# Optimization experiments

Hardware: AMD Instinct MI355X
Metric: run time of the kernel (lower is better)

Reference implementation:

```python
import jax, jax.numpy as jnp
import numpy as np

NH = 8      # num_heads
AG = 49     # agent_num
PS = 7      # pool_size = sqrt(agent_num)


def _pool_mat(in_size, out_size):
    # torch AdaptiveAvgPool2d bin boundaries: start=floor(i*n/o), end=ceil((i+1)*n/o)
    P = np.zeros((out_size, in_size), dtype=np.float32)
    for i in range(out_size):
        s = (i * in_size) // out_size
        e = -((-(i + 1) * in_size) // out_size)
        P[i, s:e] = 1.0 / (e - s)
    return jnp.asarray(P)


def setup_inputs() -> dict:
    key = jax.random.key(0)
    ks = jax.random.split(key, 16)
    b, n, dim, ic, cc = 32, 1024, 512, 512, 256
    s = 0.02
    d = {}
    d['x'] = jax.random.normal(ks[0], (b, n, dim), jnp.float32)
    d['context'] = jax.random.normal(ks[1], (b, n, cc), jnp.float32)
    d['Wq'] = jax.random.normal(ks[2], (dim, ic), jnp.float32) * s
    d['Wkv'] = jax.random.normal(ks[3], (dim, 2 * ic), jnp.float32) * s
    d['conv_w'] = jax.random.normal(ks[4], (ic, ic + cc, 3, 3), jnp.float32) * s
    d['conv_b'] = jnp.zeros((ic,), jnp.float32)
    d['dwc_w'] = jax.random.normal(ks[5], (ic, 1, 3, 3), jnp.float32) * s
    d['dwc_b'] = jnp.zeros((ic,), jnp.float32)
    d['proj_w'] = jax.random.normal(ks[6], (ic, dim), jnp.float32) * s
    d['proj_b'] = jnp.zeros((dim,), jnp.float32)
    d['an_bias'] = jax.random.normal(ks[7], (NH, AG, 7, 7), jnp.float32) * s
    d['na_bias'] = jax.random.normal(ks[8], (NH, AG, 7, 7), jnp.float32) * s
    d['ah_bias'] = jax.random.normal(ks[9], (1, NH, AG, 32, 1), jnp.float32) * s
    d['aw_bias'] = jax.random.normal(ks[10], (1, NH, AG, 1, 32), jnp.float32) * s
    d['ha_bias'] = jax.random.normal(ks[11], (1, NH, 32, 1, AG), jnp.float32) * s
    d['wa_bias'] = jax.random.normal(ks[12], (1, NH, 1, 32, AG), jnp.float32) * s
    d['H'] = 32; d['W'] = 32; d['c_H'] = 32; d['c_W'] = 32
    return d


def reference(x, context, Wq, Wkv, conv_w, conv_b, dwc_w, dwc_b, proj_w, proj_b,
              an_bias, na_bias, ah_bias, aw_bias, ha_bias, wa_bias, H, W, c_H, c_W):
    b, n, _ = x.shape
    ic = Wq.shape[1]
    cc = context.shape[-1]
    nh, ag = NH, AG
    hd = ic // nh
    scale = hd ** -0.5

    q = x @ Wq                                    # (b, n, ic)
    kv = (x @ Wkv).reshape(b, n, 2, ic)
    k, v = kv[:, :, 0], kv[:, :, 1]

    # adaptive avg pool of q and context down to (PS, PS) agent grid
    Ph, Pw = _pool_mat(H, PS), _pool_mat(W, PS)
    Pch, Pcw = _pool_mat(c_H, PS), _pool_mat(c_W, PS)
    q_img = q.reshape(b, H, W, ic).transpose(0, 3, 1, 2)            # (b, ic, H, W)
    pool_x = jnp.einsum('ph,bchw,qw->bcpq', Ph, q_img, Pw).reshape(b, ic, ag).transpose(0, 2, 1)
    c_img = context.reshape(b, c_H, c_W, cc).transpose(0, 3, 1, 2)  # (b, cc, cH, cW)
    pool_c = jnp.einsum('ph,bchw,qw->bcpq', Pch, c_img, Pcw).reshape(b, cc, ag).transpose(0, 2, 1)

    # NOTE: raw row-major reshape (b, 49, ic+cc) -> (b, ic+cc, 7, 7), exactly as in torch source
    agent = jnp.concatenate([pool_x, pool_c], axis=2).reshape(b, ic + cc, PS, PS)
    agent = jax.lax.conv_general_dilated(agent, conv_w, (1, 1), ((1, 1), (1, 1))) + conv_b[None, :, None, None]
    agent = agent.reshape(b, ic, ag)
    # NOTE: raw reshape (b, ic, 49) -> (b, 49, nh, hd), as in torch source
    a_t = agent.reshape(b, ag, nh, hd).transpose(0, 2, 1, 3)        # (b, nh, ag, hd)

    qh = q.reshape(b, n, nh, hd).transpose(0, 2, 1, 3)
    kh = k.reshape(b, n, nh, hd).transpose(0, 2, 1, 3)
    vh = v.reshape(b, n, nh, hd).transpose(0, 2, 1, 3)

    # agent -> token attention with interpolated + separable relative bias
    pb1 = jax.image.resize(an_bias, (nh, ag, H, W), 'bilinear').reshape(1, nh, ag, n)
    pb2 = (ah_bias + aw_bias).reshape(1, nh, ag, n)
    agent_attn = jax.nn.softmax(jnp.einsum('bhad,bhnd->bhan', a_t * scale, kh) + pb1 + pb2, axis=-1)
    agent_v = jnp.einsum('bhan,bhnd->bhad', agent_attn, vh)         # (b, nh, ag, hd)

    # token -> agent attention
    ab1 = jax.image.resize(na_bias, (nh, ag, H, W), 'bilinear').reshape(1, nh, ag, n).transpose(0, 1, 3, 2)
    ab2 = (ha_bias + wa_bias).reshape(1, nh, n, ag)
    q_attn = jax.nn.softmax(jnp.einsum('bhnd,bhad->bhna', qh * scale, a_t) + ab1 + ab2, axis=-1)
    out = jnp.einsum('bhna,bhad->bhnd', q_attn, agent_v).transpose(0, 2, 1, 3).reshape(b, n, ic)

    # depthwise conv positional encoding on v
    v_img = v.reshape(b, H, W, ic).transpose(0, 3, 1, 2)
    dwc = jax.lax.conv_general_dilated(v_img, dwc_w, (1, 1), ((1, 1), (1, 1)),
                                       feature_group_count=ic) + dwc_b[None, :, None, None]
    out = out + dwc.transpose(0, 2, 3, 1).reshape(b, n, ic)
    return out @ proj_w + proj_b
```

## Files before the change

### kernel.cpp

```cpp
#include <hip/hip_runtime.h>
#include <stdint.h>


typedef __attribute__((ext_vector_type(8)))  short          bf16x8;
typedef __attribute__((ext_vector_type(4)))  float          f32x4;
typedef __attribute__((ext_vector_type(4)))  unsigned short u16x4;

__device__ __forceinline__ float bf2f(unsigned short u) {
    union { unsigned int i; float f; } x; x.i = ((unsigned int)u) << 16; return x.f;
}
__device__ __forceinline__ unsigned short f2bf(float f) {
    union { float f; unsigned int i; } x; x.f = f;
    unsigned int i = x.i;
    i += 0x7FFFu + ((i >> 16) & 1u);
    return (unsigned short)(i >> 16);
}

__global__ void cvt_f32_bf16_kernel(const float* __restrict__ src,
                                    unsigned short* __restrict__ dst) {
    const int i = (blockIdx.x * 256 + threadIdx.x) * 4;
    const f32x4 v = *(const f32x4*)(src + i);
    u16x4 o; o[0]=f2bf(v[0]); o[1]=f2bf(v[1]); o[2]=f2bf(v[2]); o[3]=f2bf(v[3]);
    *(u16x4*)(dst + i) = o;
}

__global__ void build_wqkvt_kernel(const float* __restrict__ Wq,
                                   const float* __restrict__ Wkv,
                                   unsigned short* __restrict__ out) {
    const int idx = blockIdx.x * 256 + threadIdx.x;
    if (idx >= 1536*512) return;
    const int nn = idx >> 9, kk = idx & 511;
    float v = (nn < 512) ? Wq[kk*512 + nn] : Wkv[kk*1024 + (nn - 512)];
    out[idx] = f2bf(v);
}

__global__ void build_projwt_kernel(const float* __restrict__ W,
                                    unsigned short* __restrict__ out) {
    const int idx = blockIdx.x * 256 + threadIdx.x;
    if (idx >= 512*512) return;
    const int nn = idx >> 9, kk = idx & 511;
    out[idx] = f2bf(W[kk*512 + nn]);
}

__device__ __forceinline__ void bilin_coef(int i, int& i0, int& i1, float& f) {
    float pos = (i + 0.5f) * (7.0f / 32.0f) - 0.5f;
    float fl = floorf(pos);
    i0 = (int)fl; f = pos - fl;
    if (i0 < 0)       { i0 = 0; i1 = 0; f = 0.f; }
    else if (i0 >= 6) { i0 = 6; i1 = 6; f = 0.f; }
    else              { i1 = i0 + 1; }
}
__device__ __forceinline__ float bilin7(const float* __restrict__ s, int y, int x) {
    int y0,y1,x0,x1; float fy,fx;
    bilin_coef(y, y0, y1, fy); bilin_coef(x, x0, x1, fx);
    return (1.f-fy)*((1.f-fx)*s[y0*7+x0] + fx*s[y0*7+x1])
         +      fy *((1.f-fx)*s[y1*7+x0] + fx*s[y1*7+x1]);
}

__global__ void bias_prep_kernel(const float* __restrict__ an, const float* __restrict__ na,
                                 const float* __restrict__ ah, const float* __restrict__ aw,
                                 const float* __restrict__ ha, const float* __restrict__ wa,
                                 float* __restrict__ bias1, float* __restrict__ bias2) {
    int idx = blockIdx.x * 256 + threadIdx.x;
    if (idx < 8*49*1024) {
        const int nn = idx & 1023;
        const int a  = (idx >> 10) % 49;
        const int h  = idx / (49*1024);
        const int y = nn >> 5, x = nn & 31;
        float v = bilin7(an + (h*49 + a)*49, y, x)
                + ah[(h*49 + a)*32 + y] + aw[(h*49 + a)*32 + x];
        bias1[idx] = v;
    } else {
        idx -= 8*49*1024;
        if (idx >= 8*1024*49) return;
        const int a  = idx % 49;
        const int nn = (idx / 49) & 1023;
        const int h  = idx / (49*1024);
        const int y = nn >> 5, x = nn & 31;
        float v = bilin7(na + (h*49 + a)*49, y, x)
                + ha[h*1568 + y*49 + a] + wa[h*1568 + x*49 + a];
        bias2[idx] = v;
    }
}

__global__ void pool_kernel(const unsigned short* __restrict__ qkv,
                            const float* __restrict__ context,
                            float* __restrict__ pooled) {
    const int idx = blockIdx.x * 256 + threadIdx.x;
    if (idx >= 32*49*768) return;
    const int c = idx % 768;
    const int a = (idx / 768) % 49;
    const int b = idx / (768*49);
    const int p = a / 7, q = a % 7;
    const int ys = p*32/7, ye = (p*32 + 38)/7;
    const int xs = q*32/7, xe = (q*32 + 38)/7;
    float s = 0.f;
    if (c < 512) {
        for (int y = ys; y < ye; ++y)
            for (int x = xs; x < xe; ++x)
                s += bf2f(qkv[(size_t)(b*1024 + y*32 + x)*1536 + c]);
    } else {
        for (int y = ys; y < ye; ++y)
            for (int x = xs; x < xe; ++x)
                s += context[(size_t)(b*1024 + y*32 + x)*256 + (c - 512)];
    }
    pooled[idx] = s / (float)((ye - ys)*(xe - xs));
}

__global__ void im2col_kernel(const float* __restrict__ pooled,
                              unsigned short* __restrict__ i2c) {
    const int idx = blockIdx.x * 256 + threadIdx.x;
    if (idx >= 1568*6912) return;
    const int kk = idx % 6912;
    const int m  = idx / 6912;
    const int b = m / 49, spq = m % 49;
    const int p = spq / 7, q = spq % 7;
    const int ci = kk / 9, r = kk % 9;
    const int dy = r / 3, dx = r % 3;
    const int yy = p + dy - 1, xx = q + dx - 1;
    float v = 0.f;
    if (yy >= 0 && yy < 7 && xx >= 0 && xx < 7)
        v = pooled[b*37632 + ci*49 + yy*7 + xx];
    i2c[idx] = f2bf(v);
}

template <int MODE>
__launch_bounds__(256)
__global__ void gemm_nt(const unsigned short* __restrict__ A,
                        const unsigned short* __restrict__ Bt,
                        void* __restrict__ C,
                        const float* __restrict__ bias,
                        int K, int ldc, int kspan) {
    __shared__ __align__(16) unsigned char smem_raw[32768];
    unsigned short* As = (unsigned short*)smem_raw;
    unsigned short* Bs = (unsigned short*)(smem_raw + 16384);

    const int gx  = gridDim.x;
    const int gxy = gridDim.x * gridDim.y;
    const int nwg = gxy * gridDim.z;
    const int L   = (blockIdx.z * gridDim.y + blockIdx.y) * gx + blockIdx.x;
    const int qq  = nwg >> 3, rr = nwg & 7;
    const int xcd = L & 7,   ii = L >> 3;
    const int W   = (xcd < rr ? xcd * (qq + 1) : rr * (qq + 1) + (xcd - rr) * qq) + ii;
    const int bz  = W / gxy;
    const int rem = W - bz * gxy;
    const int by  = rem / gx;
    const int bx  = rem - by * gx;

    const int tid  = threadIdx.x;
    const int wid  = tid >> 6;
    const int lane = tid & 63;
    const int m0 = by * 128;
    const int n0 = bx * 128;
    const int wm = (wid >> 1) * 64;
    const int wn = (wid & 1) * 64;
    const int lrow = lane & 15;
    const int quad = lane >> 4;
    const int srow = lane >> 3;
    const int scol = ((lane & 7) ^ srow) * 8;

    f32x4 acc[4][4];
#pragma unroll
    for (int i = 0; i < 4; ++i)
#pragma unroll
        for (int j = 0; j < 4; ++j) acc[i][j] = (f32x4){0.f,0.f,0.f,0.f};

    const int kz0 = bz * kspan;
    const int kz1 = min(K, kz0 + kspan);
    for (int k0 = kz0; k0 < kz1; k0 += 64) {
        __syncthreads();
#pragma unroll
        for (int i = 0; i < 4; ++i) {
            const int chunk = wid*4 + i;
            const int row = chunk*8 + srow;
            __builtin_amdgcn_global_load_lds(
                (const __attribute__((address_space(1))) void*)(A + (size_t)(m0 + row)*K + k0 + scol),
                (__attribute__((address_space(3))) void*)(As + chunk*512), 16, 0, 0);
            __builtin_amdgcn_global_load_lds(
                (const __attribute__((address_space(1))) void*)(Bt + (size_t)(n0 + row)*K + k0 + scol),
                (__attribute__((address_space(3))) void*)(Bs + chunk*512), 16, 0, 0);
        }
        __syncthreads();
#pragma unroll
        for (int kk = 0; kk < 2; ++kk) {
            bf16x8 af[4], bfr[4];
#pragma unroll
            for (int mt = 0; mt < 4; ++mt) {
                const int row = wm + mt*16 + lrow;
                const int u = (kk*4 + quad) ^ (row & 7);
                af[mt] = *(const bf16x8*)(As + row*64 + u*8);
            }
#pragma unroll
            for (int nt = 0; nt < 4; ++nt) {
                const int row = wn + nt*16 + lrow;
                const int u = (kk*4 + quad) ^ (row & 7);
                bfr[nt] = *(const bf16x8*)(Bs + row*64 + u*8);
            }
#pragma unroll
            for (int mt = 0; mt < 4; ++mt)
#pragma unroll
                for (int nt = 0; nt < 4; ++nt)
                    acc[mt][nt] = __builtin_amdgcn_mfma_f32_16x16x32_bf16(
                        af[mt], bfr[nt], acc[mt][nt], 0, 0, 0);
        }
    }

    __syncthreads();
    if (MODE == 1) {
        unsigned short* Cs = (unsigned short*)smem_raw;
#pragma unroll
        for (int mt = 0; mt < 4; ++mt)
#pragma unroll
            for (int nt = 0; nt < 4; ++nt)
#pragma unroll
                for (int r = 0; r < 4; ++r) {
                    const int m = wm + mt*16 + quad*4 + r;
                    const int n = wn + nt*16 + lrow;
                    Cs[m*128 + (n ^ ((m & 7) << 3))] = f2bf(acc[mt][nt][r]);
                }
        __syncthreads();
#pragma unroll
        for (int it = 0; it < 8; ++it) {
            const int idx = it*256 + tid;
            const int row = idx >> 4, c8 = idx & 15;
            const bf16x8 v = *(const bf16x8*)(Cs + row*128 + ((c8*8) ^ ((row & 7) << 3)));
            *(bf16x8*)((unsigned short*)C + (size_t)(m0 + row)*ldc + n0 + c8*8) = v;
        }
    } else {
        float* Cf = (float*)smem_raw;
#pragma unroll
        for (int half = 0; half < 2; ++half) {
            if ((wid >> 1) == half) {
#pragma unroll
                for (int mt = 0; mt < 4; ++mt)
#pragma unroll
                    for (int nt = 0; nt < 4; ++nt)
#pragma unroll
                        for (int r = 0; r < 4; ++r) {
                            const int mr = mt*16 + quad*4 + r;
                            const int n  = wn + nt*16 + lrow;
                            Cf[mr*128 + (n ^ ((mr & 7) << 2))] = acc[mt][nt][r];
                        }
            }
            __syncthreads();
#pragma unroll
            for (int it = 0; it < 8; ++it) {
                const int idx = it*256 + tid;
                const int row = idx >> 5, c4 = idx & 31;
                const int m = m0 + half*64 + row;
                f32x4 v = *(const f32x4*)(Cf + row*128 + ((c4*4) ^ ((row & 7) << 2)));
                if (MODE == 0) {
                    const f32x4 bb = *(const f32x4*)(bias + n0 + c4*4);
                    v[0]+=bb[0]; v[1]+=bb[1]; v[2]+=bb[2]; v[3]+=bb[3];
                    *(f32x4*)((float*)C + (size_t)m*ldc + n0 + c4*4) = v;
                } else {
                    if (m < 1568)
                        *(f32x4*)((float*)C + ((size_t)bz*1568 + m)*512 + n0 + c4*4) = v;
                }
            }
            __syncthreads();
        }
    }
}

__global__ void convred_kernel(const float* __restrict__ part,
                               const float* __restrict__ bias,
                               unsigned short* __restrict__ at_bf) {
    const int idx = blockIdx.x * 256 + threadIdx.x;
    if (idx >= 1568*128) return;
    const int m  = idx >> 7;
    const int n4 = (idx & 127) * 4;
    f32x4 s = *(const f32x4*)&part[(size_t)m*512 + n4];
#pragma unroll
    for (int kz = 1; kz < 9; ++kz) {
        const f32x4 p = *(const f32x4*)&part[((size_t)kz*1568 + m)*512 + n4];
        s[0]+=p[0]; s[1]+=p[1]; s[2]+=p[2]; s[3]+=p[3];
    }
    u16x4 o;
    o[0] = f2bf(s[0] + bias[n4+0]);
    o[1] = f2bf(s[1] + bias[n4+1]);
    o[2] = f2bf(s[2] + bias[n4+2]);
    o[3] = f2bf(s[3] + bias[n4+3]);
    *(u16x4*)&at_bf[(size_t)m*512 + n4] = o;
}

__launch_bounds__(256)
__global__ void agent_attn_mfma_kernel(const unsigned short* __restrict__ qkv,
                                       const unsigned short* __restrict__ at_bf,
                                       const float* __restrict__ bias1,
                                       float* __restrict__ pn,
                                       float* __restrict__ pd) {
    const int bh = blockIdx.x;
    const int b = bh >> 3, h = bh & 7;
    const int sl = blockIdx.y;
    __shared__ unsigned short at_s[64*72];
    __shared__ __align__(16) unsigned char smem[4*64*72*2 + 4*64*64*2];
    unsigned short* P_s = (unsigned short*)smem;
    unsigned short* V_s = (unsigned short*)(smem + 36864);
    float* red  = (float*)smem;
    float* dred = (float*)(smem + 65536);
    const int tid  = threadIdx.x;
    const int wid  = tid >> 6, lane = tid & 63;
    const int l15  = lane & 15, quad = lane >> 4;
    const int j0   = sl*256 + wid*64;

    for (int i = tid; i < 64*72; i += 256) at_s[i] = 0;
    __syncthreads();
    for (int i = tid; i < 49*16; i += 256) {
        const int a = i >> 4, dq = (i & 15) * 4;
        *(u16x4*)&at_s[a*72 + dq] = *(const u16x4*)&at_bf[(size_t)(b*49 + a)*512 + h*64 + dq];
    }
#pragma unroll
    for (int i = 0; i < 8; ++i) {
        __builtin_amdgcn_global_load_lds(
            (const __attribute__((address_space(1))) void*)
                (qkv + (size_t)(b*1024 + j0 + i*8 + (lane>>3))*1536 + 1024 + h*64 + (lane&7)*8),
            (__attribute__((address_space(3))) void*)(V_s + wid*4096 + i*512), 16, 0, 0);
    }
    bf16x8 kfr[4][2];
#pragma unroll
    for (int nt = 0; nt < 4; ++nt)
#pragma unroll
        for (int kf = 0; kf < 2; ++kf)
            kfr[nt][kf] = *(const bf16x8*)
                (qkv + (size_t)(b*1024 + j0 + nt*16 + l15)*1536 + 512 + h*64 + kf*32 + quad*8);
    __syncthreads();

    bf16x8 af[4][2];
#pragma unroll
    for (int mt = 0; mt < 4; ++mt)
#pragma unroll
        for (int kf = 0; kf < 2; ++kf)
            af[mt][kf] = *(const bf16x8*)(at_s + (mt*16 + l15)*72 + kf*32 + quad*8);

    f32x4 acc[4][4];
#pragma unroll
    for (int i = 0; i < 4; ++i)
#pragma unroll
        for (int j = 0; j < 4; ++j) acc[i][j] = (f32x4){0.f,0.f,0.f,0.f};
#pragma unroll
    for (int kf = 0; kf < 2; ++kf)
#pragma unroll
        for (int mt = 0; mt < 4; ++mt)
#pragma unroll
            for (int nt = 0; nt < 4; ++nt)
                acc[mt][nt] = __builtin_amdgcn_mfma_f32_16x16x32_bf16(
                    af[mt][kf], kfr[nt][kf], acc[mt][nt], 0, 0, 0);

    float denp[4][4];
#pragma unroll
    for (int mt = 0; mt < 4; ++mt)
#pragma unroll
        for (int r = 0; r < 4; ++r) denp[mt][r] = 0.f;
#pragma unroll
    for (int mt = 0; mt < 4; ++mt) {
#pragma unroll
        for (int nt = 0; nt < 4; ++nt) {
#pragma unroll
            for (int r = 0; r < 4; ++r) {
                const int a  = mt*16 + quad*4 + r;
                const int ab = (a < 49) ? a : 48;
                const int jj = j0 + nt*16 + l15;
                const float e = __expf(fmaf(0.125f, acc[mt][nt][r],
                                            bias1[(h*49 + ab)*1024 + jj]));
                denp[mt][r] += e;
                P_s[wid*4608 + a*72 + nt*16 + l15] = f2bf(e);
            }
        }
    }
    __syncthreads();

    f32x4 out[4][4];
#pragma unroll
    for (int i = 0; i < 4; ++i)
#pragma unroll
        for (int j = 0; j < 4; ++j) out[i][j] = (f32x4){0.f,0.f,0.f,0.f};
#pragma unroll
    for (int kf = 0; kf < 2; ++kf) {
        bf16x8 va[4];
#pragma unroll
        for (int mt = 0; mt < 4; ++mt) {
            union { bf16x8 v; unsigned short s[8]; } u;
#pragma unroll
            for (int t = 0; t < 8; ++t)
                u.s[t] = V_s[wid*4096 + (kf*32 + quad*8 + t)*64 + mt*16 + l15];
            va[mt] = u.v;
        }
#pragma unroll
        for (int nt = 0; nt < 4; ++nt) {
            const bf16x8 pb = *(const bf16x8*)(P_s + wid*4608 + (nt*16 + l15)*72 + kf*32 + quad*8);
#pragma unroll
            for (int mt = 0; mt < 4; ++mt)
                out[mt][nt] = __builtin_amdgcn_mfma_f32_16x16x32_bf16(
                    va[mt], pb, out[mt][nt], 0, 0, 0);
        }
    }

#pragma unroll
    for (int mt = 0; mt < 4; ++mt) {
#pragma unroll
        for (int r = 0; r < 4; ++r) {
            float v = denp[mt][r];
            v += __shfl_xor(v, 1);
            v += __shfl_xor(v, 2);
            v += __shfl_xor(v, 4);
            v += __shfl_xor(v, 8);
            denp[mt][r] = v;
        }
    }

    __syncthreads();
#pragma unroll
    for (int nt = 0; nt < 4; ++nt) {
        const int a = nt*16 + l15;
#pragma unroll
        for (int mt = 0; mt < 4; ++mt)
            *(f32x4*)&red[wid*4096 + a*64 + mt*16 + quad*4] = out[mt][nt];
    }
    if (l15 == 0) {
#pragma unroll
        for (int mt = 0; mt < 4; ++mt)
#pragma unroll
            for (int r = 0; r < 4; ++r)
                dred[wid*64 + mt*16 + quad*4 + r] = denp[mt][r];
    }
    __syncthreads();
    for (int i = tid; i < 4096; i += 256) {
        const float s = red[i] + red[4096 + i] + red[8192 + i] + red[12288 + i];
        pn[((size_t)bh*4 + sl)*4096 + i] = s;
    }
    if (tid < 64) {
        const float s = dred[tid] + dred[64 + tid] + dred[128 + tid] + dred[192 + tid];
        pd[((size_t)bh*4 + sl)*64 + tid] = s;
    }
}

__global__ void agent_combine_kernel(const float* __restrict__ pn,
                                     const float* __restrict__ pd,
                                     unsigned short* __restrict__ avT) {
    const int idx = blockIdx.x * 256 + threadIdx.x;
    if (idx >= 256*4096) return;
    const int bh = idx >> 12;
    const int i  = idx & 4095;
    const int a = i >> 6, d = i & 63;
    float num = 0.f, den = 0.f;
#pragma unroll
    for (int s = 0; s < 4; ++s) {
        num += pn[(((size_t)bh*4 + s)*64 + a)*64 + d];
        den += pd[((size_t)bh*4 + s)*64 + a];
    }
    avT[(size_t)bh*4096 + d*64 + a] = (a < 49) ? f2bf(num / den) : (unsigned short)0;
}

__launch_bounds__(256)
__global__ void qattn_mfma_kernel(const unsigned short* __restrict__ qkv,
                                  const unsigned short* __restrict__ at_bf,
                                  const unsigned short* __restrict__ avT,
                                  const float* __restrict__ bias2,
                                  const float* __restrict__ dwc_w,
                                  const float* __restrict__ dwc_b,
                                  unsigned short* __restrict__ out_pre) {
    const int bh = blockIdx.x;
    const int b = bh >> 3, h = bh & 7;
    const int tq = blockIdx.y;
    __shared__ __align__(16) unsigned char smem[69632];
    unsigned short* P_s = (unsigned short*)smem;
    float* out_s = (float*)smem;
    __shared__ float dwcw_s[64*9];
    __shared__ float dwcb_s[64];
    const int tid = threadIdx.x;
    const int wid = tid >> 6, lane = tid & 63;
    const int l15 = lane & 15, quad = lane >> 4;
    const int j0  = tq*256 + wid*64;

    for (int i = tid; i < 64*9; i += 256) dwcw_s[i] = dwc_w[h*576 + i];
    if (tid < 64) dwcb_s[tid] = dwc_b[h*64 + tid];

    bf16x8 qa[4][2];
#pragma unroll
    for (int mt = 0; mt < 4; ++mt)
#pragma unroll
        for (int kf = 0; kf < 2; ++kf)
            qa[mt][kf] = *(const bf16x8*)
                (qkv + (size_t)(b*1024 + j0 + mt*16 + l15)*1536 + h*64 + kf*32 + quad*8);
    bf16x8 ab[4][2];
#pragma unroll
    for (int nt = 0; nt < 4; ++nt) {
        const int a  = nt*16 + l15;
        const int ar = (a < 49) ? a : 48;
#pragma unroll
        for (int kf = 0; kf < 2; ++kf)
            ab[nt][kf] = *(const bf16x8*)
                (at_bf + (size_t)(b*49 + ar)*512 + h*64 + kf*32 + quad*8);
    }

    f32x4 e[4][4];
#pragma unroll
    for (int i = 0; i < 4; ++i)
#pragma unroll
        for (int j = 0; j < 4; ++j) e[i][j] = (f32x4){0.f,0.f,0.f,0.f};
#pragma unroll
    for (int kf = 0; kf < 2; ++kf)
#pragma unroll
        for (int mt = 0; mt < 4; ++mt)
#pragma unroll
            for (int nt = 0; nt < 4; ++nt)
                e[mt][nt] = __builtin_amdgcn_mfma_f32_16x16x32_bf16(
                    qa[mt][kf], ab[nt][kf], e[mt][nt], 0, 0, 0);

    float denp[4][4];
#pragma unroll
    for (int mt = 0; mt < 4; ++mt)
#pragma unroll
        for (int r = 0; r < 4; ++r) denp[mt][r] = 0.f;
#pragma unroll
    for (int mt = 0; mt < 4; ++mt) {
#pragma unroll
        for (int nt = 0; nt < 4; ++nt) {
            const int a = nt*16 + l15;
#pragma unroll
            for (int r = 0; r < 4; ++r) {
                if (a < 49) {
                    const int jj = j0 + mt*16 + quad*4 + r;
                    const float v = __expf(fmaf(0.125f, e[mt][nt][r],
                                                bias2[((size_t)h*1024 + jj)*49 + a]));
                    e[mt][nt][r] = v;
                    denp[mt][r] += v;
                } else {
                    e[mt][nt][r] = 0.f;
                }
            }
        }
    }
#pragma unroll
    for (int mt = 0; mt < 4; ++mt) {
#pragma unroll
        for (int r = 0; r < 4; ++r) {
            float v = denp[mt][r];
            v += __shfl_xor(v, 1);
            v += __shfl_xor(v, 2);
            v += __shfl_xor(v, 4);
            v += __shfl_xor(v, 8);
            denp[mt][r] = 1.0f / v;
        }
    }
#pragma unroll
    for (int mt = 0; mt < 4; ++mt)
#pragma unroll
        for (int nt = 0; nt < 4; ++nt)
#pragma unroll
            for (int r = 0; r < 4; ++r)
                P_s[wid*4608 + (mt*16 + quad*4 + r)*72 + nt*16 + l15] =
                    f2bf(e[mt][nt][r] * denp[mt][r]);

    bf16x8 bv[4][2];
#pragma unroll
    for (int nt = 0; nt < 4; ++nt)
#pragma unroll
        for (int kf = 0; kf < 2; ++kf)
            bv[nt][kf] = *(const bf16x8*)
                (avT + (size_t)bh*4096 + (nt*16 + l15)*64 + kf*32 + quad*8);
    f32x4 out[4][4];
#pragma unroll
    for (int i = 0; i < 4; ++i)
#pragma unroll
        for (int j = 0; j < 4; ++j) out[i][j] = (f32x4){0.f,0.f,0.f,0.f};
#pragma unroll
    for (int kf = 0; kf < 2; ++kf) {
        bf16x8 pa[4];
#pragma unroll
        for (int mt = 0; mt < 4; ++mt)
            pa[mt] = *(const bf16x8*)(P_s + wid*4608 + (mt*16 + l15)*72 + kf*32 + quad*8);
#pragma unroll
        for (int nt = 0; nt < 4; ++nt)
#pragma unroll
            for (int mt = 0; mt < 4; ++mt)
                out[mt][nt] = __builtin_amdgcn_mfma_f32_16x16x32_bf16(
                    pa[mt], bv[nt][kf], out[mt][nt], 0, 0, 0);
    }

    __syncthreads();
#pragma unroll
    for (int mt = 0; mt < 4; ++mt)
#pragma unroll
        for (int nt = 0; nt < 4; ++nt)
#pragma unroll
            for (int r = 0; r < 4; ++r)
                out_s[(wid*64 + mt*16 + quad*4 + r)*68 + nt*16 + l15] = out[mt][nt][r];
    __syncthreads();

    const int tt = tid >> 2;
    const int p  = tid & 3;
    const int d0 = p*16;
    for (int it = 0; it < 4; ++it) {
        const int tl = it*64 + tt;
        const int jj = tq*256 + tl;
        float o[16];
#pragma unroll
        for (int i = 0; i < 16; ++i) o[i] = out_s[tl*68 + d0 + i] + dwcb_s[d0 + i];
        const int y = jj >> 5, x = jj & 31;
#pragma unroll
        for (int dy = 0; dy < 3; ++dy) {
            const int yy = y + dy - 1;
            if (yy < 0 || yy > 31) continue;
#pragma unroll
            for (int dx = 0; dx < 3; ++dx) {
                const int xx = x + dx - 1;
                if (xx < 0 || xx > 31) continue;
                const unsigned short* vp =
                    qkv + (size_t)(b*1024 + yy*32 + xx)*1536 + 1024 + h*64 + d0;
#pragma unroll
                for (int i4 = 0; i4 < 4; ++i4) {
                    const u16x4 v4 = *(const u16x4*)(vp + i4*4);
#pragma unroll
                    for (int i = 0; i < 4; ++i)
                        o[i4*4+i] = fmaf(dwcw_s[(d0 + i4*4 + i)*9 + dy*3 + dx],
                                         bf2f(v4[i]), o[i4*4+i]);
                }
            }
        }
        unsigned short* op = out_pre + (size_t)(b*1024 + jj)*512 + h*64 + d0;
#pragma unroll
        for (int i4 = 0; i4 < 4; ++i4) {
            u16x4 w;
            w[0]=f2bf(o[i4*4+0]); w[1]=f2bf(o[i4*4+1]);
            w[2]=f2bf(o[i4*4+2]); w[3]=f2bf(o[i4*4+3]);
            *(u16x4*)(op + i4*4) = w;
        }
    }
}

extern "C" void kernel_launch(void* const* d_in, const int* in_sizes, int n_in,
                              void* d_out, int out_size, void* d_ws, size_t ws_size,
                              hipStream_t stream) {
    (void)in_sizes; (void)n_in; (void)out_size; (void)ws_size;
    const float* x       = (const float*)d_in[0];
    const float* context = (const float*)d_in[1];
    const float* Wq      = (const float*)d_in[2];
    const float* Wkv     = (const float*)d_in[3];
    const float* conv_w  = (const float*)d_in[4];
    const float* conv_b  = (const float*)d_in[5];
    const float* dwc_w   = (const float*)d_in[6];
    const float* dwc_b   = (const float*)d_in[7];
    const float* proj_w  = (const float*)d_in[8];
    const float* proj_b  = (const float*)d_in[9];
    const float* an_bias = (const float*)d_in[10];
    const float* na_bias = (const float*)d_in[11];
    const float* ah_bias = (const float*)d_in[12];
    const float* aw_bias = (const float*)d_in[13];
    const float* ha_bias = (const float*)d_in[14];
    const float* wa_bias = (const float*)d_in[15];

    char* ws = (char*)d_ws;
    size_t off = 0;
    auto alloc = [&](size_t bytes) -> char* {
        char* p = ws + off; off += (bytes + 255) & ~(size_t)255; return p;
    };
    unsigned short* xb     = (unsigned short*)alloc((size_t)16777216 * 2);
    unsigned short* qkv    = (unsigned short*)alloc((size_t)50331648 * 2);
    unsigned short* wqkvt  = (unsigned short*)alloc((size_t)786432  * 2);
    unsigned short* projwt = (unsigned short*)alloc((size_t)262144  * 2);
    unsigned short* convwb = (unsigned short*)alloc((size_t)3538944 * 2);
    float*          pooled = (float*)alloc((size_t)1204224 * 4);
    unsigned short* i2c    = (unsigned short*)alloc((size_t)1664*6912*2);
    unsigned short* at_bf  = (unsigned short*)alloc((size_t)1568*512*2);
    float*          bias1  = (float*)alloc((size_t)401408 * 4);
    float*          bias2  = (float*)alloc((size_t)401408 * 4);
    unsigned short* avT    = (unsigned short*)alloc((size_t)256*4096*2);
    float*          part_conv = (float*)xb;
    float*          pn        = (float*)i2c;
    float*          pd        = pn + (size_t)256*4*64*64;
    unsigned short* outpre    = xb;

    cvt_f32_bf16_kernel<<<16384, 256, 0, stream>>>(x, xb);
    cvt_f32_bf16_kernel<<<3456, 256, 0, stream>>>(conv_w, convwb);
    build_wqkvt_kernel<<<3072, 256, 0, stream>>>(Wq, Wkv, wqkvt);
    build_projwt_kernel<<<1024, 256, 0, stream>>>(proj_w, projwt);
    bias_prep_kernel<<<3136, 256, 0, stream>>>(an_bias, na_bias, ah_bias, aw_bias,
                                               ha_bias, wa_bias, bias1, bias2);
    gemm_nt<1><<<dim3(12, 256), 256, 0, stream>>>(xb, wqkvt, qkv, nullptr, 512, 1536, 512);
    pool_kernel<<<4704, 256, 0, stream>>>(qkv, context, pooled);
    im2col_kernel<<<42336, 256, 0, stream>>>(pooled, i2c);
    gemm_nt<3><<<dim3(4, 13, 9), 256, 0, stream>>>(i2c, convwb, part_conv, nullptr, 6912, 512, 768);
    convred_kernel<<<784, 256, 0, stream>>>(part_conv, conv_b, at_bf);
    agent_attn_mfma_kernel<<<dim3(256, 4), 256, 0, stream>>>(qkv, at_bf, bias1, pn, pd);
    agent_combine_kernel<<<4096, 256, 0, stream>>>(pn, pd, avT);
    qattn_mfma_kernel<<<dim3(256, 4), 256, 0, stream>>>(qkv, at_bf, avT, bias2,
                                                        dwc_w, dwc_b, outpre);
    gemm_nt<0><<<dim3(4, 256), 256, 0, stream>>>(outpre, projwt, d_out, proj_b, 512, 512, 512);
}
```

Baseline: 487.2 us.

## Replace QKV and projection GEMMs with 256x256 double-buffered 8-wave kernel

Adds a gemm_nt8 kernel with 256x256 tiles, 8 waves, direct global-to-LDS loads into double buffers, and an interleaved schedule that stages the next tiles between four MFMA phases with setprio. It also remaps workgroups across XCDs for cache locality. It is used for the QKV projection and the output projection in place of the 128x128 gemm_nt, and the MODE 1 bf16 epilogue is removed from the old kernel. Epilogues now write straight from registers without LDS staging, which may give less coalesced stores. The larger tiles also mean fewer workgroups (768 and 256) on 256 CUs.

```diff
diff --git a/kernel.cpp b/kernel.cpp
--- a/kernel.cpp
+++ b/kernel.cpp
@@ -206,27 +206,7 @@
     }
 
     __syncthreads();
-    if (MODE == 1) {
-        unsigned short* Cs = (unsigned short*)smem_raw;
-#pragma unroll
-        for (int mt = 0; mt < 4; ++mt)
-#pragma unroll
-            for (int nt = 0; nt < 4; ++nt)
-#pragma unroll
-                for (int r = 0; r < 4; ++r) {
-                    const int m = wm + mt*16 + quad*4 + r;
-                    const int n = wn + nt*16 + lrow;
-                    Cs[m*128 + (n ^ ((m & 7) << 3))] = f2bf(acc[mt][nt][r]);
-                }
-        __syncthreads();
-#pragma unroll
-        for (int it = 0; it < 8; ++it) {
-            const int idx = it*256 + tid;
-            const int row = idx >> 4, c8 = idx & 15;
-            const bf16x8 v = *(const bf16x8*)(Cs + row*128 + ((c8*8) ^ ((row & 7) << 3)));
-            *(bf16x8*)((unsigned short*)C + (size_t)(m0 + row)*ldc + n0 + c8*8) = v;
-        }
-    } else {
+    {
         float* Cf = (float*)smem_raw;
 #pragma unroll
         for (int half = 0; half < 2; ++half) {
@@ -262,6 +242,169 @@
         }
     }
 }
+
+#define STAGE_A(DST, T, Q) do {                                                             \
+    _Pragma("unroll")                                                                       \
+    for (int l_ = 0; l_ < 2; ++l_) {                                                        \
+        const int rb_ = l_*128 + (Q)*64 + wid*8;                                            \
+        __builtin_amdgcn_global_load_lds(                                                   \
+            (const __attribute__((address_space(1))) void*)                                 \
+                (Ag + (size_t)(m0 + rb_ + lr8)*K + (T)*64 + lc8),                           \
+            (__attribute__((address_space(3))) void*)((DST) + rb_*64), 16, 0, 0);           \
+    }                                                                                       \
+} while (0)
+
+#define STAGE_B(DST, T, NH) do {                                                            \
+    _Pragma("unroll")                                                                       \
+    for (int l_ = 0; l_ < 2; ++l_) {                                                        \
+        const int w8_ = wid*8;                                                              \
+        const int rb_ = l_*128 + ((w8_ >> 5) << 6) + (NH)*32 + (w8_ & 31);                  \
+        __builtin_amdgcn_global_load_lds(                                                   \
+            (const __attribute__((address_space(1))) void*)                                 \
+                (Btg + (size_t)(n0 + rb_ + lr8)*K + (T)*64 + lc8),                          \
+            (__attribute__((address_space(3))) void*)((DST) + rb_*64), 16, 0, 0);           \
+    }                                                                                       \
+} while (0)
+
+#define LOAD_A(MH, SRC) do {                                                                \
+    _Pragma("unroll")                                                                       \
+    for (int m4_ = 0; m4_ < 4; ++m4_)                                                       \
+    _Pragma("unroll")                                                                       \
+    for (int kk_ = 0; kk_ < 2; ++kk_)                                                       \
+        aF[m4_][kk_] = *(const bf16x8*)                                                     \
+            ((SRC) + (wr*128 + ((MH)*4 + m4_)*16 + l15)*64 + kk_*32 + quad*8);              \
+} while (0)
+
+#define LOAD_B(NH, DSTF, SRC) do {                                                          \
+    _Pragma("unroll")                                                                       \
+    for (int n2_ = 0; n2_ < 2; ++n2_)                                                       \
+    _Pragma("unroll")                                                                       \
+    for (int kk_ = 0; kk_ < 2; ++kk_)                                                       \
+        DSTF[n2_][kk_] = *(const bf16x8*)                                                   \
+            ((SRC) + (wc*64 + ((NH)*2 + n2_)*16 + l15)*64 + kk_*32 + quad*8);               \
+} while (0)
+
+#define MFMA_PHASE(MH, NH, BF) do {                                                         \
+    __builtin_amdgcn_s_barrier();                                                           \
+    asm volatile("s_waitcnt lgkmcnt(0)");                                                   \
+    __builtin_amdgcn_sched_barrier(0);                                                      \
+    __builtin_amdgcn_s_setprio(1);                                                          \
+    _Pragma("unroll")                                                                       \
+    for (int kk_ = 0; kk_ < 2; ++kk_)                                                       \
+    _Pragma("unroll")                                                                       \
+    for (int m4_ = 0; m4_ < 4; ++m4_)                                                       \
+    _Pragma("unroll")                                                                       \
+    for (int n2_ = 0; n2_ < 2; ++n2_)                                                       \
+        acc[(MH)*4 + m4_][(NH)*2 + n2_] = __builtin_amdgcn_mfma_f32_16x16x32_bf16(          \
+            aF[m4_][kk_], BF[n2_][kk_], acc[(MH)*4 + m4_][(NH)*2 + n2_], 0, 0, 0);          \
+    __builtin_amdgcn_s_setprio(0);                                                          \
+    __builtin_amdgcn_sched_barrier(0);                                                      \
+} while (0)
+
+template <int MODE>
+__launch_bounds__(512, 1)
+__global__ void gemm_nt8(const unsigned short* __restrict__ Ag,
+                         const unsigned short* __restrict__ Btg,
+                         void* __restrict__ C,
+                         const float* __restrict__ bias,
+                         int K, int ldc) {
+    __shared__ unsigned short AsB[2][16384];
+    __shared__ unsigned short BsB[2][16384];
+
+    const int gx  = gridDim.x;
+    const int nwg = gx * gridDim.y;
+    const int L   = blockIdx.y * gx + blockIdx.x;
+    const int qq  = nwg >> 3, rr = nwg & 7;
+    const int xcd = L & 7,   ii = L >> 3;
+    const int W   = (xcd < rr ? xcd * (qq + 1) : rr * (qq + 1) + (xcd - rr) * qq) + ii;
+    const int bx  = W % gx, by = W / gx;
+    const int m0  = by * 256, n0 = bx * 256;
+
+    const int tid  = threadIdx.x;
+    const int wid  = tid >> 6, lane = tid & 63;
+    const int wr   = wid >> 2, wc = wid & 3;
+    const int l15  = lane & 15, quad = lane >> 4;
+    const int lr8  = lane >> 3, lc8 = (lane & 7) * 8;
+    const int KT   = K >> 6;
+
+    unsigned short *Acur = &AsB[0][0], *Anxt = &AsB[1][0];
+    unsigned short *Bcur = &BsB[0][0], *Bnxt = &BsB[1][0];
+
+    f32x4 acc[8][4];
+#pragma unroll
+    for (int i = 0; i < 8; ++i)
+#pragma unroll
+        for (int j = 0; j < 4; ++j) acc[i][j] = (f32x4){0.f,0.f,0.f,0.f};
+
+    bf16x8 aF[4][2], bF0[2][2], bF1[2][2];
+
+    STAGE_A(Acur, 0, 0); STAGE_B(Bcur, 0, 1); STAGE_A(Acur, 0, 1); STAGE_B(Bcur, 0, 0);
+    STAGE_A(Anxt, 1, 0); STAGE_B(Bnxt, 1, 1); STAGE_A(Anxt, 1, 1);
+    asm volatile("s_waitcnt vmcnt(6)");
+    __builtin_amdgcn_s_barrier();
+
+    for (int t = 0; t < KT; ++t) {
+        LOAD_B(0, bF0, Bcur);
+        LOAD_A(0, Acur);
+        if (t + 1 < KT) STAGE_B(Bnxt, t + 1, 0);
+        MFMA_PHASE(0, 0, bF0);
+        __builtin_amdgcn_s_barrier();
+
+        LOAD_B(1, bF1, Bcur);
+        if (t + 2 < KT) STAGE_A(Acur, t + 2, 0);
+        MFMA_PHASE(0, 1, bF1);
+        __builtin_amdgcn_s_barrier();
+
+        LOAD_A(1, Acur);
+        if (t + 2 < KT) STAGE_B(Bcur, t + 2, 1);
+        MFMA_PHASE(1, 1, bF1);
+        __builtin_amdgcn_s_barrier();
+
+        LOAD_B(0, bF0, Bcur);
+        if (t + 2 < KT) STAGE_A(Acur, t + 2, 1);
+        MFMA_PHASE(1, 0, bF0);
+        if (t + 2 < KT) asm volatile("s_waitcnt vmcnt(6)");
+        else            asm volatile("s_waitcnt vmcnt(0)");
+        __builtin_amdgcn_s_barrier();
+
+        unsigned short* tmp;
+        tmp = Acur; Acur = Anxt; Anxt = tmp;
+        tmp = Bcur; Bcur = Bnxt; Bnxt = tmp;
+    }
+
+    if (MODE == 1) {
+#pragma unroll
+        for (int mt = 0; mt < 8; ++mt)
+#pragma unroll
+            for (int nt = 0; nt < 4; ++nt)
+#pragma unroll
+                for (int r = 0; r < 4; ++r) {
+                    const int m = m0 + wr*128 + mt*16 + quad*4 + r;
+                    const int n = n0 + wc*64  + nt*16 + l15;
+                    ((unsigned short*)C)[(size_t)m*ldc + n] = f2bf(acc[mt][nt][r]);
+                }
+    } else {
+        float bv[4];
+#pragma unroll
+        for (int nt = 0; nt < 4; ++nt) bv[nt] = bias[n0 + wc*64 + nt*16 + l15];
+#pragma unroll
+        for (int mt = 0; mt < 8; ++mt)
+#pragma unroll
+            for (int nt = 0; nt < 4; ++nt)
+#pragma unroll
+                for (int r = 0; r < 4; ++r) {
+                    const int m = m0 + wr*128 + mt*16 + quad*4 + r;
+                    const int n = n0 + wc*64  + nt*16 + l15;
+                    ((float*)C)[(size_t)m*ldc + n] = acc[mt][nt][r] + bv[nt];
+                }
+    }
+}
+
+#undef STAGE_A
+#undef STAGE_B
+#undef LOAD_A
+#undef LOAD_B
+#undef MFMA_PHASE
 
 __global__ void convred_kernel(const float* __restrict__ part,
                                const float* __restrict__ bias,
@@ -678,7 +821,7 @@
     build_projwt_kernel<<<1024, 256, 0, stream>>>(proj_w, projwt);
     bias_prep_kernel<<<3136, 256, 0, stream>>>(an_bias, na_bias, ah_bias, aw_bias,
                                                ha_bias, wa_bias, bias1, bias2);
-    gemm_nt<1><<<dim3(12, 256), 256, 0, stream>>>(xb, wqkvt, qkv, nullptr, 512, 1536, 512);
+    gemm_nt8<1><<<dim3(6, 128), 512, 0, stream>>>(xb, wqkvt, qkv, nullptr, 512, 1536);
     pool_kernel<<<4704, 256, 0, stream>>>(qkv, context, pooled);
     im2col_kernel<<<42336, 256, 0, stream>>>(pooled, i2c);
     gemm_nt<3><<<dim3(4, 13, 9), 256, 0, stream>>>(i2c, convwb, part_conv, nullptr, 6912, 512, 768);
@@ -687,5 +830,5 @@
     agent_combine_kernel<<<4096, 256, 0, stream>>>(pn, pd, avT);
     qattn_mfma_kernel<<<dim3(256, 4), 256, 0, stream>>>(qkv, at_bf, avT, bias2,
                                                         dwc_w, dwc_b, outpre);
-    gemm_nt<0><<<dim3(4, 256), 256, 0, stream>>>(outpre, projwt, d_out, proj_b, 512, 512, 512);
-}
+    gemm_nt8<0><<<dim3(2, 128), 512, 0, stream>>>(outpre, projwt, d_out, proj_b, 512, 512);
+}
```

New measurement: 502.1 us. +3.1%, slower.
